# Performance work log

Measured on AMD Instinct MI355X. Metric: run time of the kernel, lower is better.

The kernel has to match this reference:

```python
import jax, jax.numpy as jnp
import numpy as np

N_HEADS = 16
ROPE_THETA = 10000.0


def _rope_tables(seq_len, head_dim, dtype=jnp.float32):
    half = head_dim // 2
    inv_freq = 1.0 / (ROPE_THETA ** (jnp.arange(0, half, dtype=jnp.float32) / half))
    t = jnp.arange(seq_len, dtype=jnp.float32)
    freqs = jnp.outer(t, inv_freq)  # (S, half)
    return jnp.cos(freqs).astype(dtype), jnp.sin(freqs).astype(dtype)


def _apply_rope(x, cos, sin):
    # x: (B, H, S, hd); cos/sin: (S, hd//2)
    half = x.shape[-1] // 2
    x1, x2 = x[..., :half], x[..., half:]
    c = cos[None, None, :, :]
    s = sin[None, None, :, :]
    return jnp.concatenate([x1 * c - x2 * s, x1 * s + x2 * c], axis=-1)


def setup_inputs() -> dict:
    key = jax.random.key(0)
    k1, k2, k3 = jax.random.split(key, 3)
    B, S, D = 4, 2048, 2048
    hd = D // N_HEADS
    x = jax.random.normal(k1, (B, S, D), dtype=jnp.float32)
    cos, sin = _rope_tables(S, hd)
    w_qkv = jax.random.normal(k2, (D, 3 * D), dtype=jnp.float32) * (D ** -0.5)
    w_out = jax.random.normal(k3, (D, D), dtype=jnp.float32) * (D ** -0.5)
    return {"x": x, "cos": cos, "sin": sin, "w_qkv": w_qkv, "w_out": w_out}


def reference(x, cos, sin, w_qkv, w_out):
    B, S, D = x.shape
    H = N_HEADS
    hd = D // H
    qkv = x @ w_qkv  # (B, S, 3D)
    qkv = qkv.reshape(B, S, 3, H, hd).transpose(2, 0, 3, 1, 4)  # (3, B, H, S, hd)
    q, k, v = qkv[0], qkv[1], qkv[2]
    q = _apply_rope(q, cos, sin)
    k = _apply_rope(k, cos, sin)
    scale = 1.0 / jnp.sqrt(jnp.asarray(hd, dtype=x.dtype))
    scores = jnp.einsum('bhqd,bhkd->bhqk', q, k) * scale  # (B, H, S, S)
    causal = jnp.tril(jnp.ones((S, S), dtype=bool))
    scores = jnp.where(causal[None, None, :, :], scores, jnp.asarray(-1e30, dtype=scores.dtype))
    p = jax.nn.softmax(scores, axis=-1)
    out = jnp.einsum('bhqk,bhkd->bhqd', p, v)  # (B, H, S, hd)
    out = out.transpose(0, 2, 1, 3).reshape(B, S, D)
    return out @ w_out
```

## Files before the change

### kernel.cpp

```cpp
#include <hip/hip_runtime.h>
#include <hip/hip_bf16.h>
#include <stdint.h>

typedef __bf16  bf16x8  __attribute__((ext_vector_type(8)));
typedef float   floatx4 __attribute__((ext_vector_type(4)));

typedef __attribute__((address_space(1))) void gvoid_t;
typedef __attribute__((address_space(3))) void svoid_t;

__device__ __forceinline__ void gld16(ushort* lds, const ushort* g) {
  __builtin_amdgcn_global_load_lds((gvoid_t*)g, (svoid_t*)lds, 16, 0, 0);
}

__device__ __forceinline__ ushort f2bf(float f) {
  union { float f; unsigned u; } v; v.f = f;
  unsigned u = v.u;
  return (ushort)((u + 0x7fffu + ((u >> 16) & 1u)) >> 16);
}
__device__ __forceinline__ float bf2f(ushort h) {
  union { unsigned u; float f; } v; v.u = ((unsigned)h) << 16; return v.f;
}
__device__ __forceinline__ unsigned pk2bf(float a, float b) {
  __hip_bfloat162 h = __float22bfloat162_rn(make_float2(a, b));
  union { __hip_bfloat162 h; unsigned u; } v; v.h = h; return v.u;
}

__global__ __launch_bounds__(256) void cvt_f32_bf16(
    const float* __restrict__ in, ushort* __restrict__ out) {
  int i = blockIdx.x * 256 + threadIdx.x;
  float4 a = ((const float4*)in)[i];
  ushort4 o;
  o.x = f2bf(a.x); o.y = f2bf(a.y); o.z = f2bf(a.z); o.w = f2bf(a.w);
  ((ushort4*)out)[i] = o;
}

__global__ __launch_bounds__(256) void transpose_cvt(
    const float* __restrict__ in, ushort* __restrict__ out, int R, int C) {
  __shared__ ushort tile[64][65];
  const int r0 = blockIdx.y * 64, c0 = blockIdx.x * 64;
  const int t = threadIdx.x;
#pragma unroll
  for (int rep = 0; rep < 16; rep++) {
    int idx = rep * 256 + t;
    int r = idx >> 6, c = idx & 63;
    tile[r][c] = f2bf(in[(size_t)(r0 + r) * C + c0 + c]);
  }
  __syncthreads();
#pragma unroll
  for (int rep = 0; rep < 16; rep++) {
    int idx = rep * 256 + t;
    int r = idx >> 6, c = idx & 63;
    out[(size_t)(c0 + r) * R + r0 + c] = tile[c][r];
  }
}

template <int EPI>
__global__ __launch_bounds__(512, 1) void gemm256(
    const ushort* __restrict__ A, const ushort* __restrict__ Bt,
    float* __restrict__ Cf,
    ushort* __restrict__ C0, ushort* __restrict__ C1, ushort* __restrict__ C2,
    int M, int N, int K) {
  __shared__ __align__(16) ushort As[2][2][256 * 32];
  __shared__ __align__(16) ushort Bs[2][2][256 * 32];
  const int t = threadIdx.x;
  const int lane = t & 63;
  const int w = t >> 6;
  const int l15 = lane & 15;
  const int quad = lane >> 4;
  const int m0 = blockIdx.y * 256;
  const int n0 = blockIdx.x * 256;
  const int wmB = (w >> 2) * 128;
  const int wnB = (w & 3) * 64;

  const int cS = (lane & 3) ^ ((lane >> 3) & 3);
  const size_t aoff = (size_t)(m0 + w * 32 + (lane >> 2)) * K + cS * 8;
  const size_t boff = (size_t)(n0 + w * 32 + (lane >> 2)) * K + cS * 8;

#define STAGE_A(db, kh, tile)                                                \
  { size_t ko_ = (size_t)(tile) * 64 + (kh) * 32;                            \
    gld16(&As[db][kh][w * 1024],       A + aoff + ko_);                      \
    gld16(&As[db][kh][w * 1024 + 512], A + aoff + 16 * (size_t)K + ko_); }
#define STAGE_B(db, kh, tile)                                                \
  { size_t ko_ = (size_t)(tile) * 64 + (kh) * 32;                            \
    gld16(&Bs[db][kh][w * 1024],       Bt + boff + ko_);                     \
    gld16(&Bs[db][kh][w * 1024 + 512], Bt + boff + 16 * (size_t)K + ko_); }

#define W8 asm volatile("s_waitcnt vmcnt(8)" ::: "memory");

  floatx4 acc[8][4];
  const floatx4 zero = {0.f, 0.f, 0.f, 0.f};
#pragma unroll
  for (int i = 0; i < 8; i++)
#pragma unroll
    for (int j = 0; j < 4; j++) acc[i][j] = zero;

  bf16x8 bfr[4];

#define PH(db, kh, mh, LB, STAGE, WAIT)                                        \
  {                                                                            \
    bf16x8 af[4];                                                              \
    {                                                                          \
      const ushort* Ah = &As[db][kh][0];                                       \
      _Pragma("unroll") for (int m_ = 0; m_ < 4; ++m_) {                       \
        int r_ = wmB + ((mh) * 4 + m_) * 16 + l15;                             \
        int c_ = quad ^ ((r_ >> 1) & 3);                                       \
        af[m_] = *(const bf16x8*)&Ah[r_ * 32 + c_ * 8];                        \
      }                                                                        \
      if (LB) {                                                                \
        const ushort* Bh = &Bs[db][kh][0];                                     \
        _Pragma("unroll") for (int n_ = 0; n_ < 4; ++n_) {                     \
          int r_ = wnB + n_ * 16 + l15;                                        \
          int c_ = quad ^ ((r_ >> 1) & 3);                                     \
          bfr[n_] = *(const bf16x8*)&Bh[r_ * 32 + c_ * 8];                     \
        }                                                                      \
      }                                                                        \
    }                                                                          \
    STAGE                                                                      \
    __builtin_amdgcn_s_barrier();                                              \
    asm volatile("s_waitcnt lgkmcnt(0)" ::: "memory");                         \
    __builtin_amdgcn_sched_barrier(0);                                         \
    __builtin_amdgcn_s_setprio(1);                                             \
    _Pragma("unroll") for (int m_ = 0; m_ < 4; ++m_)                           \
      _Pragma("unroll") for (int n_ = 0; n_ < 4; ++n_)                         \
        acc[(mh) * 4 + m_][n_] = __builtin_amdgcn_mfma_f32_16x16x32_bf16(      \
            af[m_], bfr[n_], acc[(mh) * 4 + m_][n_], 0, 0, 0);                 \
    __builtin_amdgcn_s_setprio(0);                                             \
    __builtin_amdgcn_sched_barrier(0);                                         \
    WAIT                                                                       \
    __builtin_amdgcn_s_barrier();                                              \
  }

  const int NT = K >> 6;
  const int NI = K >> 7;

  STAGE_A(0, 0, 0);
  STAGE_B(0, 0, 0);
  STAGE_A(0, 1, 0);
  STAGE_B(0, 1, 0);
  STAGE_A(1, 0, 1);
  STAGE_B(1, 0, 1);
  W8
  __builtin_amdgcn_s_barrier();

  for (int i = 0; i < NI; ++i) {
    const int t1 = 2 * i + 1;
    int t2 = 2 * i + 2, t3 = 2 * i + 3;
    if (t2 > NT - 1) t2 = NT - 1;
    if (t3 > NT - 1) t3 = NT - 1;
    PH(0, 0, 0, 1, STAGE_A(1, 1, t1), )
    PH(0, 0, 1, 0, STAGE_B(1, 1, t1), W8)
    PH(0, 1, 0, 1, STAGE_A(0, 0, t2), )
    PH(0, 1, 1, 0, STAGE_B(0, 0, t2), W8)
    PH(1, 0, 0, 1, STAGE_A(0, 1, t2), )
    PH(1, 0, 1, 0, STAGE_B(0, 1, t2), W8)
    PH(1, 1, 0, 1, STAGE_A(1, 0, t3), )
    PH(1, 1, 1, 0, STAGE_B(1, 0, t3), W8)
  }

#undef PH
#undef STAGE_A
#undef STAGE_B
#undef W8

  if (EPI == 0) {
#pragma unroll
    for (int m = 0; m < 8; ++m)
#pragma unroll
      for (int n = 0; n < 4; ++n)
#pragma unroll
        for (int r = 0; r < 4; ++r) {
          int row = m0 + wmB + m * 16 + quad * 4 + r;
          int col = n0 + wnB + n * 16 + l15;
          Cf[(size_t)row * N + col] = acc[m][n][r];
        }
  } else {
    const int colW = n0 + wnB;
    const int sel = colW >> 11;
    const int h = (colW >> 7) & 15;
    if (sel < 2) {
      ushort* dst = (sel == 0) ? C0 : C1;
#pragma unroll
      for (int m = 0; m < 8; ++m) {
        int rowb = m0 + wmB + m * 16 + quad * 4;
        int b = rowb >> 11, s = rowb & 2047;
#pragma unroll
        for (int n = 0; n < 4; ++n) {
          int d = (colW + n * 16 + l15) & 127;
#pragma unroll
          for (int r = 0; r < 4; ++r)
            dst[((size_t)(b * 16 + h) * 2048 + (s + r)) * 128 + d] =
                f2bf(acc[m][n][r]);
        }
      }
    } else {
#pragma unroll
      for (int m = 0; m < 8; ++m) {
        int rowb = m0 + wmB + m * 16 + quad * 4;
        int b = rowb >> 11, s = rowb & 2047;
#pragma unroll
        for (int n = 0; n < 4; ++n) {
          int d = (colW + n * 16 + l15) & 127;
          ushort4 pk;
          pk.x = f2bf(acc[m][n][0]);
          pk.y = f2bf(acc[m][n][1]);
          pk.z = f2bf(acc[m][n][2]);
          pk.w = f2bf(acc[m][n][3]);
          *(ushort4*)&C2[((size_t)(b * 16 + h) * 128 + d) * 2048 + s] = pk;
        }
      }
    }
  }
}

__global__ __launch_bounds__(256) void rope_kernel(
    ushort* __restrict__ Q, ushort* __restrict__ Kb,
    const float* __restrict__ cosT, const float* __restrict__ sinT) {
  unsigned gid = blockIdx.x * 256u + threadIdx.x;
  int d = gid & 63;
  int s = (gid >> 6) & 2047;
  int bh = (gid >> 17) & 63;
  const bool isK = (gid >> 23) != 0;
  ushort* buf = isK ? Kb : Q;
  const float sc = isK ? 1.0f
                       : 0.08838834764831845f * 1.4426950408889634f;
  size_t base = ((size_t)bh * 2048 + s) * 128;
  float x1 = bf2f(buf[base + d]);
  float x2 = bf2f(buf[base + d + 64]);
  float c = cosT[s * 64 + d];
  float sn = sinT[s * 64 + d];
  buf[base + d] = f2bf((x1 * c - x2 * sn) * sc);
  buf[base + d + 64] = f2bf((x1 * sn + x2 * c) * sc);
}

__global__ __launch_bounds__(256, 4) void attn_kernel(
    const ushort* __restrict__ Q, const ushort* __restrict__ Kb,
    const ushort* __restrict__ VT, ushort* __restrict__ O) {
  __shared__ __align__(16) ushort Ks[64 * 128];
  __shared__ __align__(16) ushort Vs[128 * 64];
  __shared__ __align__(16) ushort Ps[64 * 64];
  const int t = threadIdx.x, lane = t & 63, w = t >> 6;
  const int l15 = lane & 15, quad = lane >> 4;
  const int bid = blockIdx.x;
  const int tq = 31 - (bid >> 6);
  const int bh = bid & 63;
  const int q0 = tq * 64 + w * 16;
  const int qrow = q0 + l15;
  const size_t hbase = (size_t)bh * 2048 * 128;
  const float NEGINF = -__builtin_inff();

  bf16x8 aq[4];
#pragma unroll
  for (int kb = 0; kb < 4; kb++)
    aq[kb] = *(const bf16x8*)&Q[hbase + (size_t)qrow * 128 + kb * 32 + quad * 8];

  float m2 = NEGINF, lsum = 0.f;
  floatx4 oacc[8];
  const floatx4 zero = {0.f, 0.f, 0.f, 0.f};
#pragma unroll
  for (int dj = 0; dj < 8; dj++) oacc[dj] = zero;

  const int ntk = tq + 1;

  for (int tk = 0; tk < ntk; tk++) {
    __syncthreads();
#pragma unroll
    for (int it = 0; it < 4; it++) {
      int o = (w * 4 + it) * 64 + lane;
      {
        int row = o >> 4;
        int c = (o & 15) ^ (row & 15);
        gld16(&Ks[(w * 4 + it) * 512],
              Kb + hbase + (size_t)(tk * 64 + row) * 128 + c * 8);
      }
      {
        int row = o >> 3;
        int c = (o & 7) ^ (row & 7);
        gld16(&Vs[(w * 4 + it) * 512],
              VT + hbase + (size_t)row * 2048 + tk * 64 + c * 8);
      }
    }
    __syncthreads();

    floatx4 sacc[4];
#pragma unroll
    for (int j = 0; j < 4; j++) sacc[j] = zero;
#pragma unroll
    for (int kb = 0; kb < 4; kb++) {
#pragma unroll
      for (int j = 0; j < 4; j++) {
        int row = j * 16 + l15;
        int c = (kb * 4 + quad) ^ (row & 15);
        bf16x8 kf = *(const bf16x8*)&Ks[row * 128 + c * 8];
        sacc[j] = __builtin_amdgcn_mfma_f32_16x16x32_bf16(kf, aq[kb], sacc[j],
                                                          0, 0, 0);
      }
    }

    if (tk == tq) {
#pragma unroll
      for (int j = 0; j < 4; j++)
#pragma unroll
        for (int r = 0; r < 4; r++) {
          int kcol = tk * 64 + j * 16 + quad * 4 + r;
          if (kcol > qrow) sacc[j][r] = NEGINF;
        }
    }

    float mx = sacc[0][0];
#pragma unroll
    for (int j = 0; j < 4; j++)
#pragma unroll
      for (int r = 0; r < 4; r++) mx = fmaxf(mx, sacc[j][r]);
    mx = fmaxf(mx, __shfl_xor(mx, 16));
    mx = fmaxf(mx, __shfl_xor(mx, 32));
    float mnew = fmaxf(m2, mx);
    float alpha = __builtin_exp2f(m2 - mnew);
    m2 = mnew;
    float rs = 0.f;
#pragma unroll
    for (int j = 0; j < 4; j++)
#pragma unroll
      for (int r = 0; r < 4; r++) {
        float p = __builtin_exp2f(sacc[j][r] - mnew);
        sacc[j][r] = p;
        rs += p;
      }
    rs += __shfl_xor(rs, 16);
    rs += __shfl_xor(rs, 32);
    lsum = lsum * alpha + rs;
    if (__any(alpha < 1.0f)) {
#pragma unroll
      for (int dj = 0; dj < 8; dj++) oacc[dj] *= alpha;
    }

#pragma unroll
    for (int j = 0; j < 4; j++) {
      unsigned lo = pk2bf(sacc[j][0], sacc[j][1]);
      unsigned hi = pk2bf(sacc[j][2], sacc[j][3]);
      int g = j * 2 + (quad >> 1);
      int gp = g ^ (l15 & 7);
      uint2 pv; pv.x = lo; pv.y = hi;
      *(uint2*)&Ps[(w * 16 + l15) * 64 + gp * 8 + (quad & 1) * 4] = pv;
    }

    bf16x8 bp[2];
#pragma unroll
    for (int kk = 0; kk < 2; kk++) {
      int g = kk * 4 + quad;
      int gp = g ^ (l15 & 7);
      bp[kk] = *(const bf16x8*)&Ps[(w * 16 + l15) * 64 + gp * 8];
    }
#pragma unroll
    for (int kk = 0; kk < 2; kk++)
#pragma unroll
      for (int dj = 0; dj < 8; dj++) {
        int rowd = dj * 16 + l15;
        int c = (kk * 4 + quad) ^ (rowd & 7);
        bf16x8 av = *(const bf16x8*)&Vs[rowd * 64 + c * 8];
        oacc[dj] = __builtin_amdgcn_mfma_f32_16x16x32_bf16(av, bp[kk], oacc[dj],
                                                           0, 0, 0);
      }
  }

  const int b = bh >> 4, h = bh & 15;
  const float rl = 1.0f / lsum;
  const size_t obase = ((size_t)(b * 2048 + qrow)) * 2048 + h * 128;
#pragma unroll
  for (int dj = 0; dj < 8; dj++) {
    ushort4 pk;
    pk.x = f2bf(oacc[dj][0] * rl);
    pk.y = f2bf(oacc[dj][1] * rl);
    pk.z = f2bf(oacc[dj][2] * rl);
    pk.w = f2bf(oacc[dj][3] * rl);
    *(ushort4*)&O[obase + dj * 16 + quad * 4] = pk;
  }
}

extern "C" void kernel_launch(void* const* d_in, const int* in_sizes, int n_in,
                              void* d_out, int out_size, void* d_ws, size_t ws_size,
                              hipStream_t stream) {
  const float* x    = (const float*)d_in[0];
  const float* cosT = (const float*)d_in[1];
  const float* sinT = (const float*)d_in[2];
  const float* wqkv = (const float*)d_in[3];
  const float* wout = (const float*)d_in[4];
  float* out = (float*)d_out;
  char* ws = (char*)d_ws;

  ushort* xbf   = (ushort*)d_out;
  ushort* wqkvT = (ushort*)(ws);
  ushort* Ob    = (ushort*)(ws);
  ushort* woutT = (ushort*)(ws + 33554432);
  ushort* Qb    = (ushort*)(ws + 41943040);
  ushort* Kbuf  = (ushort*)(ws + 75497472);
  ushort* VTb   = (ushort*)(ws + 109051904);

  cvt_f32_bf16<<<16384, 256, 0, stream>>>(x, xbf);
  transpose_cvt<<<dim3(96, 32), 256, 0, stream>>>(wqkv, wqkvT, 2048, 6144);
  transpose_cvt<<<dim3(32, 32), 256, 0, stream>>>(wout, woutT, 2048, 2048);
  gemm256<1><<<dim3(24, 32), 512, 0, stream>>>(xbf, wqkvT, nullptr,
                                               Qb, Kbuf, VTb, 8192, 6144, 2048);
  rope_kernel<<<65536, 256, 0, stream>>>(Qb, Kbuf, cosT, sinT);
  attn_kernel<<<2048, 256, 0, stream>>>(Qb, Kbuf, VTb, Ob);
  gemm256<0><<<dim3(8, 32), 512, 0, stream>>>(Ob, woutT, out,
                                              nullptr, nullptr, nullptr,
                                              8192, 2048, 2048);
}
```

Before: 620.5 us.

## Double-buffer A fragments and prefetch next phase's LDS reads during MFMA

After: 600.2 us. -3.3%, faster.

```diff
diff --git a/kernel.cpp b/kernel.cpp
--- a/kernel.cpp
+++ b/kernel.cpp
@@ -76,6 +76,23 @@
   const size_t aoff = (size_t)(m0 + w * 32 + (lane >> 2)) * K + cS * 8;
   const size_t boff = (size_t)(n0 + w * 32 + (lane >> 2)) * K + cS * 8;
 
+  const ushort* const Ab = &As[0][0][0];
+  const ushort* const Bb = &Bs[0][0][0];
+  const ushort* aP[4];
+  const ushort* bP[4];
+#pragma unroll
+  for (int m = 0; m < 4; ++m) {
+    int r = wmB + m * 16 + l15;
+    int c = quad ^ ((r >> 1) & 3);
+    aP[m] = Ab + r * 32 + c * 8;
+  }
+#pragma unroll
+  for (int n = 0; n < 4; ++n) {
+    int r = wnB + n * 16 + l15;
+    int c = quad ^ ((r >> 1) & 3);
+    bP[n] = Bb + r * 32 + c * 8;
+  }
+
 #define STAGE_A(db, kh, tile)                                                \
   { size_t ko_ = (size_t)(tile) * 64 + (kh) * 32;                            \
     gld16(&As[db][kh][w * 1024],       A + aoff + ko_);                      \
@@ -85,7 +102,13 @@
     gld16(&Bs[db][kh][w * 1024],       Bt + boff + ko_);                     \
     gld16(&Bs[db][kh][w * 1024 + 512], Bt + boff + 16 * (size_t)K + ko_); }
 
-#define W8 asm volatile("s_waitcnt vmcnt(8)" ::: "memory");
+#define LDA(AF, db, kh, mh)                                                  \
+  _Pragma("unroll") for (int m_ = 0; m_ < 4; ++m_)                           \
+    AF[m_] = *(const bf16x8*)(aP[m_] +                                       \
+                              ((db) * 16384 + (kh) * 8192 + (mh) * 2048));
+#define LDB(db, kh)                                                          \
+  _Pragma("unroll") for (int n_ = 0; n_ < 4; ++n_)                           \
+    bfr[n_] = *(const bf16x8*)(bP[n_] + ((db) * 16384 + (kh) * 8192));
 
   floatx4 acc[8][4];
   const floatx4 zero = {0.f, 0.f, 0.f, 0.f};
@@ -94,41 +117,23 @@
 #pragma unroll
     for (int j = 0; j < 4; j++) acc[i][j] = zero;
 
-  bf16x8 bfr[4];
-
-#define PH(db, kh, mh, LB, STAGE, WAIT)                                        \
-  {                                                                            \
-    bf16x8 af[4];                                                              \
-    {                                                                          \
-      const ushort* Ah = &As[db][kh][0];                                       \
-      _Pragma("unroll") for (int m_ = 0; m_ < 4; ++m_) {                       \
-        int r_ = wmB + ((mh) * 4 + m_) * 16 + l15;                             \
-        int c_ = quad ^ ((r_ >> 1) & 3);                                       \
-        af[m_] = *(const bf16x8*)&Ah[r_ * 32 + c_ * 8];                        \
-      }                                                                        \
-      if (LB) {                                                                \
-        const ushort* Bh = &Bs[db][kh][0];                                     \
-        _Pragma("unroll") for (int n_ = 0; n_ < 4; ++n_) {                     \
-          int r_ = wnB + n_ * 16 + l15;                                        \
-          int c_ = quad ^ ((r_ >> 1) & 3);                                     \
-          bfr[n_] = *(const bf16x8*)&Bh[r_ * 32 + c_ * 8];                     \
-        }                                                                      \
-      }                                                                        \
-    }                                                                          \
-    STAGE                                                                      \
-    __builtin_amdgcn_s_barrier();                                              \
-    asm volatile("s_waitcnt lgkmcnt(0)" ::: "memory");                         \
-    __builtin_amdgcn_sched_barrier(0);                                         \
-    __builtin_amdgcn_s_setprio(1);                                             \
-    _Pragma("unroll") for (int m_ = 0; m_ < 4; ++m_)                           \
-      _Pragma("unroll") for (int n_ = 0; n_ < 4; ++n_)                         \
-        acc[(mh) * 4 + m_][n_] = __builtin_amdgcn_mfma_f32_16x16x32_bf16(      \
-            af[m_], bfr[n_], acc[(mh) * 4 + m_][n_], 0, 0, 0);                 \
-    __builtin_amdgcn_s_setprio(0);                                             \
-    __builtin_amdgcn_sched_barrier(0);                                         \
-    WAIT                                                                       \
-    __builtin_amdgcn_s_barrier();                                              \
-  }
+  bf16x8 af0[4], af1[4], bfr[4];
+
+#define PH(db, kh, mh, AFU, AFL, ndb, nkh, nmh, STAGE)                       \
+  __builtin_amdgcn_s_barrier();                                              \
+  if ((mh) == 0) { LDB(db, kh) }                                             \
+  asm volatile("s_waitcnt lgkmcnt(0)" ::: "memory");                         \
+  __builtin_amdgcn_sched_barrier(0);                                         \
+  __builtin_amdgcn_s_setprio(1);                                             \
+  _Pragma("unroll") for (int m_ = 0; m_ < 4; ++m_)                           \
+    _Pragma("unroll") for (int n_ = 0; n_ < 4; ++n_)                         \
+      acc[(mh) * 4 + m_][n_] = __builtin_amdgcn_mfma_f32_16x16x32_bf16(      \
+          AFU[m_], bfr[n_], acc[(mh) * 4 + m_][n_], 0, 0, 0);                \
+  __builtin_amdgcn_s_setprio(0);                                             \
+  __builtin_amdgcn_sched_barrier(0);                                         \
+  LDA(AFL, ndb, nkh, nmh)                                                    \
+  STAGE                                                                      \
+  asm volatile("s_waitcnt vmcnt(8)" ::: "memory");
 
   const int NT = K >> 6;
   const int NI = K >> 7;
@@ -139,28 +144,31 @@
   STAGE_B(0, 1, 0);
   STAGE_A(1, 0, 1);
   STAGE_B(1, 0, 1);
-  W8
+  asm volatile("s_waitcnt vmcnt(4)" ::: "memory");
   __builtin_amdgcn_s_barrier();
+  LDA(af0, 0, 0, 0)
 
   for (int i = 0; i < NI; ++i) {
     const int t1 = 2 * i + 1;
     int t2 = 2 * i + 2, t3 = 2 * i + 3;
     if (t2 > NT - 1) t2 = NT - 1;
     if (t3 > NT - 1) t3 = NT - 1;
-    PH(0, 0, 0, 1, STAGE_A(1, 1, t1), )
-    PH(0, 0, 1, 0, STAGE_B(1, 1, t1), W8)
-    PH(0, 1, 0, 1, STAGE_A(0, 0, t2), )
-    PH(0, 1, 1, 0, STAGE_B(0, 0, t2), W8)
-    PH(1, 0, 0, 1, STAGE_A(0, 1, t2), )
-    PH(1, 0, 1, 0, STAGE_B(0, 1, t2), W8)
-    PH(1, 1, 0, 1, STAGE_A(1, 0, t3), )
-    PH(1, 1, 1, 0, STAGE_B(1, 0, t3), W8)
-  }
+    PH(0, 0, 0, af0, af1, 0, 0, 1, STAGE_A(1, 1, t1))
+    PH(0, 0, 1, af1, af0, 0, 1, 0, STAGE_B(1, 1, t1))
+    PH(0, 1, 0, af0, af1, 0, 1, 1, STAGE_A(0, 0, t2))
+    PH(0, 1, 1, af1, af0, 1, 0, 0, STAGE_B(0, 0, t2))
+    PH(1, 0, 0, af0, af1, 1, 0, 1, STAGE_A(0, 1, t2))
+    PH(1, 0, 1, af1, af0, 1, 1, 0, STAGE_B(0, 1, t2))
+    PH(1, 1, 0, af0, af1, 1, 1, 1, STAGE_A(1, 0, t3))
+    PH(1, 1, 1, af1, af0, 0, 0, 0, STAGE_B(1, 0, t3))
+  }
+  asm volatile("s_waitcnt vmcnt(0)" ::: "memory");
 
 #undef PH
+#undef LDA
+#undef LDB
 #undef STAGE_A
 #undef STAGE_B
-#undef W8
 
   if (EPI == 0) {
 #pragma unroll
```
